# Kernel tuning notes

Measured on AMD Instinct MI355X. Metric: run time of the kernel, lower is better.

## Reference

```python
import jax, jax.numpy as jnp
import numpy as np

N = 3072          # num nodes
H = 256           # hidden_features
B = 4             # num_heads
HD = H // B       # per-head dim
PRIOR_MU = 1.0
PRIOR_SIGMA = 1.0
LN_EPS = 1e-5


def setup_inputs() -> dict:
    key = jax.random.key(0)
    ks = jax.random.split(key, 12)
    s = 0.02  # weight init scale
    return {
        "h": jax.random.normal(ks[0], (N, H), jnp.float32),
        "gamma": jnp.ones((H,), jnp.float32),
        "beta": jnp.zeros((H,), jnp.float32),
        "W_k": jax.random.normal(ks[1], (H, H), jnp.float32) * s,
        "b_k": jnp.zeros((H,), jnp.float32),
        "W_mu": jax.random.normal(ks[2], (H, H), jnp.float32) * s,
        "b_mu": jnp.zeros((H,), jnp.float32),
        "W_ls": jax.random.normal(ks[3], (H, H), jnp.float32) * s,
        "b_ls": jnp.zeros((H,), jnp.float32),
        "W_v": jax.random.normal(ks[4], (H * B, H), jnp.float32) * s,
        "b_v": jnp.zeros((H,), jnp.float32),
        "diffusion": jax.random.uniform(ks[5], (N, N, 1), jnp.float32),
        "eps": jax.random.normal(ks[6], (N, N, B), jnp.float32),
    }


def reference(h, gamma, beta, W_k, b_k, W_mu, b_mu, W_ls, b_ls, W_v, b_v, diffusion, eps):
    h0 = h
    # LayerNorm
    mean = jnp.mean(h, axis=-1, keepdims=True)
    var = jnp.var(h, axis=-1, keepdims=True)
    hn = (h - mean) * jax.lax.rsqrt(var + LN_EPS) * gamma + beta
    # Q/K-style projections, split into heads: [N, HD, B]
    k = (hn @ W_k + b_k).reshape(N, HD, B)
    mu = (hn @ W_mu + b_mu).reshape(N, HD, B)
    ls = (hn @ W_ls + b_ls).reshape(N, HD, B)
    scale = HD ** -0.5
    mu = jnp.einsum('xyb,zyb->xzb', k, mu) * scale       # [N, N, B]
    ls = jnp.einsum('xyb,zyb->xzb', k, ls) * scale       # [N, N, B]
    sigma = jax.nn.softplus(ls)
    # KL(LogNormal(mu, sigma) || LogNormal(log(prior_mu), prior_sigma))
    mu_p = jnp.log(jnp.asarray(PRIOR_MU, h.dtype))
    sig_p = jnp.asarray(PRIOR_SIGMA, h.dtype)
    kl = (jnp.log(sig_p / sigma)
          + (sigma ** 2 + (mu - mu_p) ** 2) / (2.0 * sig_p ** 2)
          - 0.5)
    kl = (kl * jnp.sign(diffusion)).sum(-1).mean()
    # reparameterized LogNormal sample, masked by diffusion matrix
    a = jnp.exp(mu + sigma * eps) * diffusion            # [N, N, B]
    # L1 normalize over source-node axis (dim=-2), torch F.normalize semantics
    denom = jnp.clip(jnp.sum(jnp.abs(a), axis=-2, keepdims=True), 1e-12)
    a = a / denom
    # diffusion-weighted aggregation: [N, B, H] -> [N, B*H]
    out = jnp.einsum('xyb,yz->xbz', a, hn).reshape(N, B * H)
    out = out @ W_v + b_v                                 # fc_v (dropout = eval mode)
    out = jax.nn.elu(out) + h0
    return out, kl
```

## Files before the change

### kernel.cpp

```cpp
#include <hip/hip_runtime.h>
#include <hip/hip_bf16.h>


#define NN 3072
#define HH 256
#define NB 4
#define HD 64
constexpr int SP = 4;
constexpr int ZCHUNK = NN / SP;
constexpr int ZT = 32;
constexpr int NIT = ZCHUNK / ZT;
constexpr int KMLSZ = 192 * 2 * 64 * 8;

typedef __attribute__((ext_vector_type(8))) short bf16x8;
typedef __attribute__((ext_vector_type(4))) float f32x4;

static __device__ inline short f2bf(float f) {
    __hip_bfloat16 h = __float2bfloat16(f);
    return __builtin_bit_cast(short, h);
}

__global__ void k0_prep(const float* __restrict__ Wk, const float* __restrict__ Wmu,
                        const float* __restrict__ Wls, const float* __restrict__ bk,
                        const float* __restrict__ bmu, const float* __restrict__ bls,
                        const float* __restrict__ Wv, short* __restrict__ WTcat,
                        float* __restrict__ biascat, short* __restrict__ WvT,
                        float* __restrict__ denom) {
    __shared__ float t[64][65];
    int bx = blockIdx.x;
    if (bx < 48) {
        int mat = bx >> 4;
        int by = (bx >> 2) & 3, bc = bx & 3;
        int y0 = by * 64, c0 = bc * 64;
        const float* W = (mat == 0) ? Wk : (mat == 1 ? Wmu : Wls);
        float scale = (mat == 0) ? 0.125f : 1.f;
        int r = threadIdx.x >> 4, c4 = (threadIdx.x & 15) * 4;
#pragma unroll
        for (int i = 0; i < 4; i++) {
            int yl = r + i * 16;
            float4 v = *(const float4*)(W + (y0 + yl) * 256 + c0 + c4);
            t[yl][c4] = v.x; t[yl][c4 + 1] = v.y; t[yl][c4 + 2] = v.z; t[yl][c4 + 3] = v.w;
        }
        __syncthreads();
#pragma unroll
        for (int i = 0; i < 4; i++) {
            int cl = r + i * 16;
            int corig = c0 + cl;
            int cp = mat * 256 + (corig & 3) * 64 + (corig >> 2);
            short4 v = make_short4(f2bf(t[c4][cl] * scale), f2bf(t[c4 + 1][cl] * scale),
                                   f2bf(t[c4 + 2][cl] * scale), f2bf(t[c4 + 3][cl] * scale));
            *(short4*)(WTcat + cp * 256 + y0 + c4) = v;
        }
        return;
    }
    if (bx < 112) {
        int b = bx - 48;
        int bk2 = b >> 2, bn = b & 3;
        int k0 = bk2 * 64, n0 = bn * 64;
        int r = threadIdx.x >> 4, c4 = (threadIdx.x & 15) * 4;
#pragma unroll
        for (int i = 0; i < 4; i++) {
            int kk = r + i * 16;
            float4 v = *(const float4*)(Wv + (k0 + kk) * 256 + n0 + c4);
            t[kk][c4] = v.x; t[kk][c4 + 1] = v.y; t[kk][c4 + 2] = v.z; t[kk][c4 + 3] = v.w;
        }
        __syncthreads();
#pragma unroll
        for (int i = 0; i < 4; i++) {
            int nn = r + i * 16;
            short4 v = make_short4(f2bf(t[c4][nn]), f2bf(t[c4 + 1][nn]),
                                   f2bf(t[c4 + 2][nn]), f2bf(t[c4 + 3][nn]));
            *(short4*)(WvT + (n0 + nn) * 1024 + k0 + c4) = v;
        }
        return;
    }
    if (bx == 112) {
        int cc = threadIdx.x;
        int corig = (cc & 63) * 4 + (cc >> 6);
        biascat[cc] = bk[corig] * 0.125f;
        biascat[256 + cc] = bmu[corig];
        biascat[512 + cc] = bls[corig];
        return;
    }
    int i = (bx - 113) * 256 + threadIdx.x;
    if (i < 13312) denom[i] = 0.f;
}

__global__ void k1_ln(const float* __restrict__ h, const float* __restrict__ gamma,
                      const float* __restrict__ beta, short* __restrict__ hn) {
    int row = blockIdx.x, tid = threadIdx.x;
    float v = h[row * 256 + tid];
    float s = v, s2 = v * v;
    for (int off = 32; off; off >>= 1) {
        s += __shfl_xor(s, off);
        s2 += __shfl_xor(s2, off);
    }
    __shared__ float red[8];
    int w = tid >> 6, lane = tid & 63;
    if (!lane) { red[w] = s; red[4 + w] = s2; }
    __syncthreads();
    s = red[0] + red[1] + red[2] + red[3];
    s2 = red[4] + red[5] + red[6] + red[7];
    float mean = s * (1.f / 256.f);
    float var = s2 * (1.f / 256.f) - mean * mean;
    float rs = rsqrtf(var + 1e-5f);
    hn[row * 256 + tid] = f2bf((v - mean) * rs * gamma[tid] + beta[tid]);
}

__global__ void k1b_tr(const short* __restrict__ hn, short* __restrict__ hnT) {
    __shared__ short t[64][68];
    int bn = blockIdx.x >> 2, bh = blockIdx.x & 3;
    int n0 = bn * 64, h0 = bh * 64;
    int r = threadIdx.x >> 4, c4 = (threadIdx.x & 15) * 4;
#pragma unroll
    for (int i = 0; i < 4; i++) {
        int nn = r + i * 16;
        *(short4*)&t[nn][c4] = *(const short4*)(hn + (n0 + nn) * 256 + h0 + c4);
    }
    __syncthreads();
#pragma unroll
    for (int i = 0; i < 4; i++) {
        int hh = r + i * 16;
        short4 v = make_short4(t[c4][hh], t[c4 + 1][hh], t[c4 + 2][hh], t[c4 + 3][hh]);
        *(short4*)(hnT + (h0 + hh) * NN + n0 + c4) = v;
    }
}

__global__ __launch_bounds__(256) void k2_proj(const short* __restrict__ hn,
                                               const short* __restrict__ WTcat,
                                               const float* __restrict__ biascat,
                                               short* __restrict__ kml) {
    int bx = blockIdx.x;
    int mt = bx / 12, nb = bx % 12;
    int m0 = mt * 64, n0 = nb * 64;
    int tid = threadIdx.x, w = tid >> 6, lane = tid & 63, q = lane >> 4, c = lane & 15;
    int mrow = m0 + w * 16;
    f32x4 acc[4] = {{0, 0, 0, 0}, {0, 0, 0, 0}, {0, 0, 0, 0}, {0, 0, 0, 0}};
    for (int k0 = 0; k0 < 256; k0 += 32) {
        bf16x8 af = *(const bf16x8*)(hn + (mrow + c) * 256 + k0 + q * 8);
#pragma unroll
        for (int nt = 0; nt < 4; nt++) {
            bf16x8 bf = *(const bf16x8*)(WTcat + (n0 + nt * 16 + c) * 256 + k0 + q * 8);
            acc[nt] = __builtin_amdgcn_mfma_f32_16x16x32_bf16(af, bf, acc[nt], 0, 0, 0);
        }
    }
#pragma unroll
    for (int nt = 0; nt < 4; nt++) {
        int cp = n0 + nt * 16 + c;
        float bias = biascat[cp];
        int mat = cp >> 8, b = (cp >> 6) & 3, y = cp & 63;
        short* dst = kml + (size_t)(mat * 4 + b) * KMLSZ;
        int kh2 = y >> 5, lq = (y >> 3) & 3, j = y & 7;
        int zt = mt * 4 + w;
#pragma unroll
        for (int r = 0; r < 4; r++) {
            int ml = 4 * q + r;
            dst[(((zt * 2 + kh2) * 64) + lq * 16 + ml) * 8 + j] = f2bf(acc[nt][r] + bias);
        }
    }
}

__global__ __launch_bounds__(256) void k3_fused(
    const short* __restrict__ kml, const short* __restrict__ hnT,
    const float* __restrict__ eps, const float* __restrict__ diff,
    float* __restrict__ aggp, float* __restrict__ denom, float* __restrict__ klsum) {
    __shared__ float eps_s[4][32][20];
    __shared__ float diff_s[32][20];
    __shared__ short hnT_s[16 * 64 * 8];
    __shared__ short a_s[4][16][40];
    __shared__ float klred[4];

    const int tid = threadIdx.x;
    const int w = tid >> 6;
    const int lane = tid & 63;
    const int q = lane >> 4;
    const int c = lane & 15;

    const int xt = blockIdx.x >> 2;
    const int sp = blockIdx.x & 3;
    const int x0 = xt * 16;
    const int zbase = sp * ZCHUNK;

    const short* khp = kml + (size_t)(0 * 4 + w) * KMLSZ;
    const short* mup = kml + (size_t)(1 * 4 + w) * KMLSZ;
    const short* lsp = kml + (size_t)(2 * 4 + w) * KMLSZ;

    const bf16x8 qf0 = *(const bf16x8*)(khp + ((xt * 2 + 0) * 64 + lane) * 8);
    const bf16x8 qf1 = *(const bf16x8*)(khp + ((xt * 2 + 1) * 64 + lane) * 8);

    f32x4 acc[16];
#pragma unroll
    for (int i = 0; i < 16; i++) acc[i] = (f32x4){0.f, 0.f, 0.f, 0.f};
    float den_acc = 0.f, kl_acc = 0.f;

    int xx[2], zz[2];
#pragma unroll
    for (int i = 0; i < 2; i++) { int p = i * 256 + tid; xx[i] = p >> 5; zz[i] = p & 31; }

    f32x4 e_reg[2];
    float d_reg[2];
    bf16x8 hp_reg[4];
#pragma unroll
    for (int i = 0; i < 2; i++) {
        int base = (x0 + xx[i]) * NN + zbase + zz[i];
        e_reg[i] = __builtin_nontemporal_load((const f32x4*)(eps + (size_t)base * 4));
        d_reg[i] = __builtin_nontemporal_load(diff + base);
    }
#pragma unroll
    for (int i = 0; i < 4; i++)
        hp_reg[i] = *(const bf16x8*)(hnT + (size_t)(w * 64 + i * 16 + c) * NN + zbase + q * 8);

    for (int it = 0; it < NIT; ++it) {
        const int z0 = zbase + it * ZT;
        __syncthreads();
#pragma unroll
        for (int i = 0; i < 2; i++) {
            eps_s[0][zz[i]][xx[i]] = e_reg[i].x;
            eps_s[1][zz[i]][xx[i]] = e_reg[i].y;
            eps_s[2][zz[i]][xx[i]] = e_reg[i].z;
            eps_s[3][zz[i]][xx[i]] = e_reg[i].w;
            diff_s[zz[i]][xx[i]] = d_reg[i];
        }
#pragma unroll
        for (int i = 0; i < 4; i++)
            *(bf16x8*)(&hnT_s[((w * 4 + i) * 64 + lane) * 8]) = hp_reg[i];
        __syncthreads();

        if (it + 1 < NIT) {
            const int z1 = z0 + ZT;
#pragma unroll
            for (int i = 0; i < 2; i++) {
                int base = (x0 + xx[i]) * NN + z1 + zz[i];
                e_reg[i] = __builtin_nontemporal_load((const f32x4*)(eps + (size_t)base * 4));
                d_reg[i] = __builtin_nontemporal_load(diff + base);
            }
#pragma unroll
            for (int i = 0; i < 4; i++)
                hp_reg[i] = *(const bf16x8*)(hnT + (size_t)(w * 64 + i * 16 + c) * NN + z1 + q * 8);
        }

        const int zt0 = (zbase >> 4) + it * 2;
        f32x4 smu[2], sls[2];
#pragma unroll
        for (int t = 0; t < 2; t++) {
            bf16x8 a0 = *(const bf16x8*)(mup + (((zt0 + t) * 2 + 0) * 64 + lane) * 8);
            bf16x8 a1 = *(const bf16x8*)(mup + (((zt0 + t) * 2 + 1) * 64 + lane) * 8);
            f32x4 z4 = (f32x4){0.f, 0.f, 0.f, 0.f};
            z4 = __builtin_amdgcn_mfma_f32_16x16x32_bf16(a0, qf0, z4, 0, 0, 0);
            z4 = __builtin_amdgcn_mfma_f32_16x16x32_bf16(a1, qf1, z4, 0, 0, 0);
            smu[t] = z4;
            bf16x8 b0 = *(const bf16x8*)(lsp + (((zt0 + t) * 2 + 0) * 64 + lane) * 8);
            bf16x8 b1 = *(const bf16x8*)(lsp + (((zt0 + t) * 2 + 1) * 64 + lane) * 8);
            f32x4 y4 = (f32x4){0.f, 0.f, 0.f, 0.f};
            y4 = __builtin_amdgcn_mfma_f32_16x16x32_bf16(b0, qf0, y4, 0, 0, 0);
            y4 = __builtin_amdgcn_mfma_f32_16x16x32_bf16(b1, qf1, y4, 0, 0, 0);
            sls[t] = y4;
        }

#pragma unroll
        for (int t = 0; t < 2; t++) {
            short pk[4];
#pragma unroll
            for (int r = 0; r < 4; r++) {
                int zl = t * 16 + 4 * q + r;
                float mu = smu[t][r];
                float ls = sls[t][r];
                float e = eps_s[w][zl][c];
                float d = diff_s[zl][c];
                float ex = __expf(-fabsf(ls));
                float sg = fmaxf(ls, 0.f) + __logf(1.f + ex);
                float kle = -__logf(sg) + 0.5f * (sg * sg + mu * mu) - 0.5f;
                float sgn = (d > 0.f) ? 1.f : ((d < 0.f) ? -1.f : 0.f);
                kl_acc += sgn * kle;
                float a = __expf(mu + sg * e) * d;
                den_acc += fabsf(a);
                pk[r] = f2bf(a);
            }
            *reinterpret_cast<short4*>(&a_s[w][c][t * 16 + 4 * q]) =
                make_short4(pk[0], pk[1], pk[2], pk[3]);
        }
        bf16x8 af = *(const bf16x8*)(&a_s[w][c][q * 8]);
#pragma unroll
        for (int nt = 0; nt < 16; nt++) {
            bf16x8 bfr = *(const bf16x8*)(&hnT_s[(nt * 64 + lane) * 8]);
            acc[nt] = __builtin_amdgcn_mfma_f32_16x16x32_bf16(af, bfr, acc[nt], 0, 0, 0);
        }
    }

    den_acc += __shfl_down(den_acc, 32);
    den_acc += __shfl_down(den_acc, 16);
    if (q == 0) atomicAdd(&denom[(x0 + c) * NB + w], den_acc);
    for (int off = 32; off; off >>= 1) kl_acc += __shfl_xor(kl_acc, off);
    if (lane == 0) klred[w] = kl_acc;
    __syncthreads();
    if (tid == 0) atomicAdd(klsum, klred[0] + klred[1] + klred[2] + klred[3]);

    float* dst = aggp + (size_t)sp * (NN * NB * HH);
#pragma unroll
    for (int nt = 0; nt < 16; nt++)
#pragma unroll
        for (int r = 0; r < 4; r++)
            dst[((size_t)(x0 + 4 * q + r) * NB + w) * HH + nt * 16 + c] = acc[nt][r];
}

__global__ void k35_norm(const float* __restrict__ aggp, const float* __restrict__ denom,
                         short* __restrict__ aggn) {
    int x = blockIdx.x, tid = threadIdx.x;
    int b = tid >> 6;
    int h4 = (tid & 63) * 4;
    size_t base = ((size_t)x * 4 + b) * 256 + h4;
    float4 s = {0.f, 0.f, 0.f, 0.f};
#pragma unroll
    for (int sp = 0; sp < SP; sp++) {
        float4 v = *(const float4*)(aggp + (size_t)sp * (NN * 4 * 256) + base);
        s.x += v.x; s.y += v.y; s.z += v.z; s.w += v.w;
    }
    float r = 1.f / fmaxf(denom[x * 4 + b], 1e-12f);
    short4 o = make_short4(f2bf(s.x * r), f2bf(s.y * r), f2bf(s.z * r), f2bf(s.w * r));
    *(short4*)(aggn + base) = o;
}

__global__ __launch_bounds__(256) void k4_out(const short* __restrict__ aggn,
                                              const short* __restrict__ WvT,
                                              const float* __restrict__ bv,
                                              const float* __restrict__ h,
                                              const float* __restrict__ klsum,
                                              float* __restrict__ out) {
    int bx = blockIdx.x;
    int mt = bx >> 2, nb = bx & 3;
    int m0 = mt * 64, n0 = nb * 64;
    int tid = threadIdx.x, w = tid >> 6, lane = tid & 63, q = lane >> 4, c = lane & 15;
    int mrow = m0 + w * 16;
    f32x4 acc[4] = {{0, 0, 0, 0}, {0, 0, 0, 0}, {0, 0, 0, 0}, {0, 0, 0, 0}};
    for (int k0 = 0; k0 < 1024; k0 += 32) {
        bf16x8 af = *(const bf16x8*)(aggn + (mrow + c) * 1024 + k0 + q * 8);
#pragma unroll
        for (int nt = 0; nt < 4; nt++) {
            bf16x8 bf = *(const bf16x8*)(WvT + (n0 + nt * 16 + c) * 1024 + k0 + q * 8);
            acc[nt] = __builtin_amdgcn_mfma_f32_16x16x32_bf16(af, bf, acc[nt], 0, 0, 0);
        }
    }
#pragma unroll
    for (int nt = 0; nt < 4; nt++) {
        int col = n0 + nt * 16 + c;
        float bias = bv[col];
#pragma unroll
        for (int r = 0; r < 4; r++) {
            int row = mrow + 4 * q + r;
            float v = acc[nt][r] + bias;
            v = (v > 0.f) ? v : (__expf(v) - 1.f);
            out[row * 256 + col] = v + h[row * 256 + col];
        }
    }
    if (bx == 0 && tid == 0) out[786432] = klsum[0] * (1.0f / 9437184.0f);
}

extern "C" void kernel_launch(void* const* d_in, const int* in_sizes, int n_in,
                              void* d_out, int out_size, void* d_ws, size_t ws_size,
                              hipStream_t stream) {
    const float* h = (const float*)d_in[0];
    const float* gamma = (const float*)d_in[1];
    const float* beta = (const float*)d_in[2];
    const float* Wk = (const float*)d_in[3];
    const float* bk = (const float*)d_in[4];
    const float* Wmu = (const float*)d_in[5];
    const float* bmu = (const float*)d_in[6];
    const float* Wls = (const float*)d_in[7];
    const float* bls = (const float*)d_in[8];
    const float* Wv = (const float*)d_in[9];
    const float* bv = (const float*)d_in[10];
    const float* diff = (const float*)d_in[11];
    const float* eps = (const float*)d_in[12];
    float* out = (float*)d_out;

    char* p = (char*)d_ws;
    float* aggp = (float*)p;   p += (size_t)SP * 12582912;
    float* denom = (float*)p;  p += 49152;
    float* klsum = (float*)p;  p += 4096;
    short* hn = (short*)p;     p += 1572864;
    short* hnT = (short*)p;    p += 1572864;
    short* kml = (short*)p;    p += 4718592;
    short* WTcat = (short*)p;  p += 393216;
    float* biasc = (float*)p;  p += 4096;
    short* WvT = (short*)p;    p += 524288;
    short* aggn = (short*)p;

    k0_prep<<<165, 256, 0, stream>>>(Wk, Wmu, Wls, bk, bmu, bls, Wv, WTcat, biasc, WvT,
                                     denom);
    k1_ln<<<3072, 256, 0, stream>>>(h, gamma, beta, hn);
    k1b_tr<<<192, 256, 0, stream>>>(hn, hnT);
    k2_proj<<<576, 256, 0, stream>>>(hn, WTcat, biasc, kml);
    k3_fused<<<192 * SP, 256, 0, stream>>>(kml, hnT, eps, diff, aggp, denom, klsum);
    k35_norm<<<3072, 256, 0, stream>>>(aggp, denom, aggn);
    k4_out<<<192, 256, 0, stream>>>(aggn, WvT, bv, h, klsum, out);
}
```

Baseline: 470.8 us.

## Split fused attention kernel into elementwise pass and tiled bf16 GEMM aggregation

Replaces the single fused kernel, which computed the attention weights and aggregated them against hn on the fly, with two kernels. The first computes the attention matrix a (bf16) for all heads and writes it to a 72MB workspace along with denom and KL. The second runs a double-buffered, LDS-swizzled GEMM that uses global_load_lds for a·hnT, with a 2-way K split. This gives better MFMA reuse in the aggregation, at the cost of writing and then re-reading a large intermediate through HBM plus an extra launch.

```diff
diff --git a/kernel.cpp b/kernel.cpp
--- a/kernel.cpp
+++ b/kernel.cpp
@@ -6,10 +6,9 @@
 #define HH 256
 #define NB 4
 #define HD 64
-constexpr int SP = 4;
-constexpr int ZCHUNK = NN / SP;
-constexpr int ZT = 32;
-constexpr int NIT = ZCHUNK / ZT;
+constexpr int KS = 2;
+constexpr int CZ = 256;
+constexpr int NCH = NN / CZ;
 constexpr int KMLSZ = 192 * 2 * 64 * 8;
 
 typedef __attribute__((ext_vector_type(8))) short bf16x8;
@@ -18,6 +17,12 @@
 static __device__ inline short f2bf(float f) {
     __hip_bfloat16 h = __float2bfloat16(f);
     return __builtin_bit_cast(short, h);
+}
+
+typedef const __attribute__((address_space(1))) unsigned int* gas_ptr;
+typedef __attribute__((address_space(3))) unsigned int* las_ptr;
+static __device__ inline void gload_lds16(const void* g, void* l) {
+    __builtin_amdgcn_global_load_lds((gas_ptr)g, (las_ptr)l, 16, 0, 0);
 }
 
 __global__ void k0_prep(const float* __restrict__ Wk, const float* __restrict__ Wmu,
@@ -160,147 +165,177 @@
     }
 }
 
-__global__ __launch_bounds__(256) void k3_fused(
-    const short* __restrict__ kml, const short* __restrict__ hnT,
-    const float* __restrict__ eps, const float* __restrict__ diff,
-    float* __restrict__ aggp, float* __restrict__ denom, float* __restrict__ klsum) {
-    __shared__ float eps_s[4][32][20];
-    __shared__ float diff_s[32][20];
-    __shared__ short hnT_s[16 * 64 * 8];
-    __shared__ short a_s[4][16][40];
+__global__ __launch_bounds__(256) void k3a_elem(
+    const short* __restrict__ kml, const float* __restrict__ eps,
+    const float* __restrict__ diff, short* __restrict__ a,
+    float* __restrict__ denom, float* __restrict__ klsum) {
     __shared__ float klred[4];
-
     const int tid = threadIdx.x;
-    const int w = tid >> 6;
-    const int lane = tid & 63;
-    const int q = lane >> 4;
-    const int c = lane & 15;
-
-    const int xt = blockIdx.x >> 2;
-    const int sp = blockIdx.x & 3;
+    const int w = tid >> 6, lane = tid & 63, q = lane >> 4, c = lane & 15;
+    const int xt = blockIdx.x % 192;
+    const int ch = blockIdx.x / 192;
     const int x0 = xt * 16;
-    const int zbase = sp * ZCHUNK;
-
-    const short* khp = kml + (size_t)(0 * 4 + w) * KMLSZ;
-    const short* mup = kml + (size_t)(1 * 4 + w) * KMLSZ;
-    const short* lsp = kml + (size_t)(2 * 4 + w) * KMLSZ;
-
-    const bf16x8 qf0 = *(const bf16x8*)(khp + ((xt * 2 + 0) * 64 + lane) * 8);
-    const bf16x8 qf1 = *(const bf16x8*)(khp + ((xt * 2 + 1) * 64 + lane) * 8);
-
-    f32x4 acc[16];
-#pragma unroll
-    for (int i = 0; i < 16; i++) acc[i] = (f32x4){0.f, 0.f, 0.f, 0.f};
-    float den_acc = 0.f, kl_acc = 0.f;
-
-    int xx[2], zz[2];
-#pragma unroll
-    for (int i = 0; i < 2; i++) { int p = i * 256 + tid; xx[i] = p >> 5; zz[i] = p & 31; }
-
-    f32x4 e_reg[2];
-    float d_reg[2];
-    bf16x8 hp_reg[4];
-#pragma unroll
-    for (int i = 0; i < 2; i++) {
-        int base = (x0 + xx[i]) * NN + zbase + zz[i];
-        e_reg[i] = __builtin_nontemporal_load((const f32x4*)(eps + (size_t)base * 4));
-        d_reg[i] = __builtin_nontemporal_load(diff + base);
-    }
-#pragma unroll
-    for (int i = 0; i < 4; i++)
-        hp_reg[i] = *(const bf16x8*)(hnT + (size_t)(w * 64 + i * 16 + c) * NN + zbase + q * 8);
-
-    for (int it = 0; it < NIT; ++it) {
-        const int z0 = zbase + it * ZT;
-        __syncthreads();
-#pragma unroll
-        for (int i = 0; i < 2; i++) {
-            eps_s[0][zz[i]][xx[i]] = e_reg[i].x;
-            eps_s[1][zz[i]][xx[i]] = e_reg[i].y;
-            eps_s[2][zz[i]][xx[i]] = e_reg[i].z;
-            eps_s[3][zz[i]][xx[i]] = e_reg[i].w;
-            diff_s[zz[i]][xx[i]] = d_reg[i];
-        }
-#pragma unroll
-        for (int i = 0; i < 4; i++)
-            *(bf16x8*)(&hnT_s[((w * 4 + i) * 64 + lane) * 8]) = hp_reg[i];
-        __syncthreads();
-
-        if (it + 1 < NIT) {
-            const int z1 = z0 + ZT;
-#pragma unroll
-            for (int i = 0; i < 2; i++) {
-                int base = (x0 + xx[i]) * NN + z1 + zz[i];
-                e_reg[i] = __builtin_nontemporal_load((const f32x4*)(eps + (size_t)base * 4));
-                d_reg[i] = __builtin_nontemporal_load(diff + base);
-            }
-#pragma unroll
-            for (int i = 0; i < 4; i++)
-                hp_reg[i] = *(const bf16x8*)(hnT + (size_t)(w * 64 + i * 16 + c) * NN + z1 + q * 8);
-        }
-
-        const int zt0 = (zbase >> 4) + it * 2;
-        f32x4 smu[2], sls[2];
-#pragma unroll
-        for (int t = 0; t < 2; t++) {
-            bf16x8 a0 = *(const bf16x8*)(mup + (((zt0 + t) * 2 + 0) * 64 + lane) * 8);
-            bf16x8 a1 = *(const bf16x8*)(mup + (((zt0 + t) * 2 + 1) * 64 + lane) * 8);
-            f32x4 z4 = (f32x4){0.f, 0.f, 0.f, 0.f};
-            z4 = __builtin_amdgcn_mfma_f32_16x16x32_bf16(a0, qf0, z4, 0, 0, 0);
-            z4 = __builtin_amdgcn_mfma_f32_16x16x32_bf16(a1, qf1, z4, 0, 0, 0);
-            smu[t] = z4;
-            bf16x8 b0 = *(const bf16x8*)(lsp + (((zt0 + t) * 2 + 0) * 64 + lane) * 8);
-            bf16x8 b1 = *(const bf16x8*)(lsp + (((zt0 + t) * 2 + 1) * 64 + lane) * 8);
-            f32x4 y4 = (f32x4){0.f, 0.f, 0.f, 0.f};
-            y4 = __builtin_amdgcn_mfma_f32_16x16x32_bf16(b0, qf0, y4, 0, 0, 0);
-            y4 = __builtin_amdgcn_mfma_f32_16x16x32_bf16(b1, qf1, y4, 0, 0, 0);
-            sls[t] = y4;
-        }
-
-#pragma unroll
-        for (int t = 0; t < 2; t++) {
+    const int zw = ch * CZ + w * 64;
+
+    bf16x8 qf[NB][2];
+#pragma unroll
+    for (int b = 0; b < NB; b++)
+#pragma unroll
+        for (int kh = 0; kh < 2; kh++)
+            qf[b][kh] = *(const bf16x8*)(kml + (size_t)b * KMLSZ +
+                                         ((xt * 2 + kh) * 64 + lane) * 8);
+
+    float den_acc[NB] = {0.f, 0.f, 0.f, 0.f};
+    float kl_acc = 0.f;
+    const size_t xrow = (size_t)(x0 + c) * NN;
+
+#pragma unroll
+    for (int t = 0; t < 4; t++) {
+        const int z = zw + t * 16;
+        const int zt2 = z >> 4;
+        f32x4 e4[4];
+        float dif[4];
+#pragma unroll
+        for (int r = 0; r < 4; r++) {
+            e4[r] = *(const f32x4*)(eps + (xrow + (size_t)(z + 4 * q + r)) * 4);
+            dif[r] = diff[xrow + z + 4 * q + r];
+        }
+#pragma unroll
+        for (int b = 0; b < NB; b++) {
+            const short* mup = kml + (size_t)(NB + b) * KMLSZ;
+            const short* lsp = kml + (size_t)(2 * NB + b) * KMLSZ;
+            bf16x8 a0 = *(const bf16x8*)(mup + ((zt2 * 2 + 0) * 64 + lane) * 8);
+            bf16x8 a1 = *(const bf16x8*)(mup + ((zt2 * 2 + 1) * 64 + lane) * 8);
+            f32x4 smu = {0.f, 0.f, 0.f, 0.f};
+            smu = __builtin_amdgcn_mfma_f32_16x16x32_bf16(a0, qf[b][0], smu, 0, 0, 0);
+            smu = __builtin_amdgcn_mfma_f32_16x16x32_bf16(a1, qf[b][1], smu, 0, 0, 0);
+            bf16x8 l0 = *(const bf16x8*)(lsp + ((zt2 * 2 + 0) * 64 + lane) * 8);
+            bf16x8 l1 = *(const bf16x8*)(lsp + ((zt2 * 2 + 1) * 64 + lane) * 8);
+            f32x4 sls = {0.f, 0.f, 0.f, 0.f};
+            sls = __builtin_amdgcn_mfma_f32_16x16x32_bf16(l0, qf[b][0], sls, 0, 0, 0);
+            sls = __builtin_amdgcn_mfma_f32_16x16x32_bf16(l1, qf[b][1], sls, 0, 0, 0);
             short pk[4];
 #pragma unroll
             for (int r = 0; r < 4; r++) {
-                int zl = t * 16 + 4 * q + r;
-                float mu = smu[t][r];
-                float ls = sls[t][r];
-                float e = eps_s[w][zl][c];
-                float d = diff_s[zl][c];
+                float mu = smu[r];
+                float ls = sls[r];
+                float e = e4[r][b];
+                float d = dif[r];
                 float ex = __expf(-fabsf(ls));
                 float sg = fmaxf(ls, 0.f) + __logf(1.f + ex);
                 float kle = -__logf(sg) + 0.5f * (sg * sg + mu * mu) - 0.5f;
                 float sgn = (d > 0.f) ? 1.f : ((d < 0.f) ? -1.f : 0.f);
                 kl_acc += sgn * kle;
-                float a = __expf(mu + sg * e) * d;
-                den_acc += fabsf(a);
-                pk[r] = f2bf(a);
+                float av = __expf(mu + sg * e) * d;
+                den_acc[b] += fabsf(av);
+                pk[r] = f2bf(av);
             }
-            *reinterpret_cast<short4*>(&a_s[w][c][t * 16 + 4 * q]) =
+            *(short4*)(a + ((size_t)b * NN + x0 + c) * NN + z + 4 * q) =
                 make_short4(pk[0], pk[1], pk[2], pk[3]);
         }
-        bf16x8 af = *(const bf16x8*)(&a_s[w][c][q * 8]);
-#pragma unroll
-        for (int nt = 0; nt < 16; nt++) {
-            bf16x8 bfr = *(const bf16x8*)(&hnT_s[(nt * 64 + lane) * 8]);
-            acc[nt] = __builtin_amdgcn_mfma_f32_16x16x32_bf16(af, bfr, acc[nt], 0, 0, 0);
-        }
-    }
-
-    den_acc += __shfl_down(den_acc, 32);
-    den_acc += __shfl_down(den_acc, 16);
-    if (q == 0) atomicAdd(&denom[(x0 + c) * NB + w], den_acc);
+    }
+#pragma unroll
+    for (int b = 0; b < NB; b++) {
+        float d = den_acc[b];
+        d += __shfl_down(d, 32);
+        d += __shfl_down(d, 16);
+        if (q == 0) atomicAdd(&denom[(x0 + c) * NB + b], d);
+    }
     for (int off = 32; off; off >>= 1) kl_acc += __shfl_xor(kl_acc, off);
     if (lane == 0) klred[w] = kl_acc;
     __syncthreads();
     if (tid == 0) atomicAdd(klsum, klred[0] + klred[1] + klred[2] + klred[3]);
-
-    float* dst = aggp + (size_t)sp * (NN * NB * HH);
-#pragma unroll
-    for (int nt = 0; nt < 16; nt++)
-#pragma unroll
-        for (int r = 0; r < 4; r++)
-            dst[((size_t)(x0 + 4 * q + r) * NB + w) * HH + nt * 16 + c] = acc[nt][r];
+}
+
+__global__ __launch_bounds__(256) void k3b_agg(
+    const short* __restrict__ a, const short* __restrict__ hnT,
+    float* __restrict__ aggp) {
+    __shared__ short As[2][64 * 64];
+    __shared__ short Bs[2][256 * 64];
+    const int tid = threadIdx.x;
+    const int w = tid >> 6, lane = tid & 63, q = lane >> 4, c = lane & 15;
+    const int bid = blockIdx.x;
+    const int b = bid & 3;
+    const int ksp = (bid >> 2) & 1;
+    const int m0 = (bid >> 3) * 64;
+    const int kbase = ksp * (NN / KS);
+
+    const char* Ag = (const char*)(a + ((size_t)b * NN + m0) * NN + kbase);
+    const char* Bg = (const char*)(hnT + kbase);
+
+    f32x4 acc[4][4];
+#pragma unroll
+    for (int i = 0; i < 4; i++)
+#pragma unroll
+        for (int j = 0; j < 4; j++) acc[i][j] = (f32x4){0.f, 0.f, 0.f, 0.f};
+
+    auto stage = [&](int buf, int ks) {
+        const int kb = ks * 128;
+#pragma unroll
+        for (int l = 0; l < 2; l++) {
+            int idx = l * 256 + tid;
+            int row = idx >> 3;
+            int colb = ((idx & 7) * 16) ^ ((row & 7) << 4);
+            gload_lds16(Ag + (size_t)row * (NN * 2) + kb + colb,
+                        (char*)&As[buf][0] + idx * 16);
+        }
+#pragma unroll
+        for (int l = 0; l < 8; l++) {
+            int idx = l * 256 + tid;
+            int row = idx >> 3;
+            int colb = ((idx & 7) * 16) ^ ((row & 7) << 4);
+            gload_lds16(Bg + (size_t)row * (NN * 2) + kb + colb,
+                        (char*)&Bs[buf][0] + idx * 16);
+        }
+    };
+
+    stage(0, 0);
+    int cur = 0;
+    for (int ks = 0; ks < NN / KS / 64; ks++) {
+        __syncthreads();
+        if (ks + 1 < NN / KS / 64) stage(cur ^ 1, ks + 1);
+        bf16x8 af[4][2], bf[4][2];
+#pragma unroll
+        for (int mt = 0; mt < 4; mt++) {
+            int row = mt * 16 + c;
+#pragma unroll
+            for (int kh = 0; kh < 2; kh++) {
+                int col = (kh * 64 + q * 16) ^ ((row & 7) << 4);
+                af[mt][kh] = *(const bf16x8*)((const char*)&As[cur][0] + row * 128 + col);
+            }
+        }
+#pragma unroll
+        for (int nt = 0; nt < 4; nt++) {
+            int row = w * 64 + nt * 16 + c;
+#pragma unroll
+            for (int kh = 0; kh < 2; kh++) {
+                int col = (kh * 64 + q * 16) ^ ((row & 7) << 4);
+                bf[nt][kh] = *(const bf16x8*)((const char*)&Bs[cur][0] + row * 128 + col);
+            }
+        }
+#pragma unroll
+        for (int mt = 0; mt < 4; mt++)
+#pragma unroll
+            for (int nt = 0; nt < 4; nt++) {
+                acc[mt][nt] = __builtin_amdgcn_mfma_f32_16x16x32_bf16(
+                    af[mt][0], bf[nt][0], acc[mt][nt], 0, 0, 0);
+                acc[mt][nt] = __builtin_amdgcn_mfma_f32_16x16x32_bf16(
+                    af[mt][1], bf[nt][1], acc[mt][nt], 0, 0, 0);
+            }
+        cur ^= 1;
+    }
+
+    float* dst = aggp + (size_t)ksp * (NN * NB * HH);
+#pragma unroll
+    for (int mt = 0; mt < 4; mt++)
+#pragma unroll
+        for (int nt = 0; nt < 4; nt++)
+#pragma unroll
+            for (int r = 0; r < 4; r++) {
+                int x = m0 + mt * 16 + 4 * q + r;
+                int n = w * 64 + nt * 16 + c;
+                dst[(size_t)x * 1024 + b * 256 + n] = acc[mt][nt][r];
+            }
 }
 
 __global__ void k35_norm(const float* __restrict__ aggp, const float* __restrict__ denom,
@@ -311,7 +346,7 @@
     size_t base = ((size_t)x * 4 + b) * 256 + h4;
     float4 s = {0.f, 0.f, 0.f, 0.f};
 #pragma unroll
-    for (int sp = 0; sp < SP; sp++) {
+    for (int sp = 0; sp < KS; sp++) {
         float4 v = *(const float4*)(aggp + (size_t)sp * (NN * 4 * 256) + base);
         s.x += v.x; s.y += v.y; s.z += v.z; s.w += v.w;
     }
@@ -374,7 +409,8 @@
     float* out = (float*)d_out;
 
     char* p = (char*)d_ws;
-    float* aggp = (float*)p;   p += (size_t)SP * 12582912;
+    short* a = (short*)p;      p += (size_t)75497472;
+    float* aggp = (float*)p;   p += (size_t)KS * 12582912;
     float* denom = (float*)p;  p += 49152;
     float* klsum = (float*)p;  p += 4096;
     short* hn = (short*)p;     p += 1572864;
@@ -390,7 +426,8 @@
     k1_ln<<<3072, 256, 0, stream>>>(h, gamma, beta, hn);
     k1b_tr<<<192, 256, 0, stream>>>(hn, hnT);
     k2_proj<<<576, 256, 0, stream>>>(hn, WTcat, biasc, kml);
-    k3_fused<<<192 * SP, 256, 0, stream>>>(kml, hnT, eps, diff, aggp, denom, klsum);
+    k3a_elem<<<192 * NCH, 256, 0, stream>>>(kml, eps, diff, a, denom, klsum);
+    k3b_agg<<<48 * NB * KS, 256, 0, stream>>>(a, hnT, aggp);
     k35_norm<<<3072, 256, 0, stream>>>(aggp, denom, aggn);
     k4_out<<<192, 256, 0, stream>>>(aggn, WvT, bv, h, klsum, out);
 }
```

Measured after the change: 437.4 us. 1.08x faster.
